# Kernel tuning notes

Hardware: AMD Instinct MI355X
Metric: run time of the kernel (lower is better)

## Reference

```python
import jax, jax.numpy as jnp
import numpy as np

B, BOUNDS, NRIM, K, UNITS = 4096, 512, 6, 4, 600
H_IN, DK_IN, DV_IN = 4, 64, 400
H_C, DK_C, DV_C = 4, 32, 100


def setup_inputs() -> dict:
    key = jax.random.key(0)
    ks = jax.random.split(key, 16)
    s = 0.02
    return {
        'inputs': jax.random.normal(ks[0], (B, BOUNDS + NRIM), jnp.float32),
        'hs': jax.random.normal(ks[1], (B, NRIM, UNITS), jnp.float32) * s,
        'cs': jax.random.normal(ks[2], (B, NRIM, UNITS), jnp.float32) * s,
        'Wk': jax.random.normal(ks[3], (BOUNDS, H_IN * DK_IN), jnp.float32) * s,
        'bk': jnp.zeros((H_IN * DK_IN,), jnp.float32),
        'Wv': jax.random.normal(ks[4], (BOUNDS, H_IN * DV_IN), jnp.float32) * s,
        'bv': jnp.zeros((H_IN * DV_IN,), jnp.float32),
        'Wq': jax.random.normal(ks[5], (NRIM, UNITS, H_IN * DK_IN), jnp.float32) * s,
        'lstm_k': jax.random.normal(ks[6], (NRIM, DV_IN, 4 * UNITS), jnp.float32) * s,
        'lstm_r': jax.random.normal(ks[7], (NRIM, UNITS, 4 * UNITS), jnp.float32) * s,
        'lstm_b': jnp.zeros((NRIM, 4 * UNITS), jnp.float32),
        'Wkc': jax.random.normal(ks[8], (NRIM, UNITS, H_C * DK_C), jnp.float32) * s,
        'Wvc': jax.random.normal(ks[9], (NRIM, UNITS, H_C * DV_C), jnp.float32) * s,
        'Wqc': jax.random.normal(ks[10], (NRIM, UNITS, H_C * DK_C), jnp.float32) * s,
        'Wout': jax.random.normal(ks[11], (NRIM, H_C * DV_C, UNITS), jnp.float32) * s,
    }


def _split_heads(t, n_heads, d_head):
    # [B, T, n_heads*d_head] -> [B, n_heads, T, d_head] (matches tf.split+stack)
    b, t_len = t.shape[0], t.shape[1]
    return t.reshape(b, t_len, n_heads, d_head).transpose(0, 2, 1, 3)


def reference(inputs, hs, cs, Wk, bk, Wv, bv, Wq, lstm_k, lstm_r, lstm_b, Wkc, Wvc, Wqc, Wout):
    x = inputs[:, :BOUNDS]                                   # [B, bounds]
    rim_dist = inputs[:, BOUNDS:BOUNDS + NRIM]               # [B, nRIM]

    # ---- input attention ----
    xx = jnp.stack([x, jnp.zeros_like(x)], axis=1)           # [B, 2, bounds]
    k_lay = xx @ Wk + bk                                     # [B, 2, H*dk]
    v_lay = xx @ Wv + bv                                     # [B, 2, H*dv]
    q_lay = jnp.einsum('bnu,nuo->bno', hs, Wq)               # grouped linear [B, nRIM, H*dq]
    kh = _split_heads(k_lay, H_IN, DK_IN)                    # [B, H, 2, dk]
    vh = _split_heads(v_lay, H_IN, DV_IN)                    # [B, H, 2, dv]
    qh = _split_heads(q_lay, H_IN, DK_IN)                    # [B, H, nRIM, dk]
    v2 = vh.mean(axis=1)                                     # [B, 2, dv]
    scores = jnp.einsum('bhnd,bhtd->bhnt', qh, kh) / np.sqrt(DK_IN).astype(np.float32)
    scores2 = scores.mean(axis=1)                            # [B, nRIM, 2]

    # top-k RIM selection mask from RIM_dist (use_attn=False path)
    _, idx = jax.lax.top_k(rim_dist, K)                      # [B, K]
    mask = jnp.zeros((inputs.shape[0], NRIM), inputs.dtype)
    mask = mask.at[jnp.arange(inputs.shape[0])[:, None], idx].set(1.0)[..., None]  # [B, nRIM, 1]

    probs = jax.nn.softmax(scores2, axis=-1)                 # dropout inactive (training=False)
    rnn_in = jnp.einsum('bnt,btv->bnv', probs, v2) * mask    # [B, nRIM, dv]

    # ---- grouped LSTM (keras gate order i,f,c,o) ----
    gates = (jnp.einsum('bnv,nvo->bno', rnn_in, lstm_k)
             + jnp.einsum('bnu,nuo->bno', hs, lstm_r) + lstm_b)  # [B, nRIM, 4*units]
    i, f, g, o = jnp.split(gates, 4, axis=-1)
    c_rnn = jax.nn.sigmoid(f) * cs + jax.nn.sigmoid(i) * jnp.tanh(g)
    h_rnn = jax.nn.sigmoid(o) * jnp.tanh(c_rnn)
    h_new = jax.lax.stop_gradient(h_rnn * (1.0 - mask)) + h_rnn * mask

    # ---- communication attention among RIMs ----
    kc = _split_heads(jnp.einsum('bnu,nuo->bno', h_new, Wkc), H_C, DK_C)  # [B, Hc, nRIM, dkc]
    vc = _split_heads(jnp.einsum('bnu,nuo->bno', h_new, Wvc), H_C, DV_C)
    qc = _split_heads(jnp.einsum('bnu,nuo->bno', h_new, Wqc), H_C, DK_C)
    sc = jnp.einsum('bhnd,bhmd->bhnm', qc, kc) / np.sqrt(DK_C).astype(np.float32)
    pc = jax.nn.softmax(sc, axis=-1) * mask[:, None, :, :]   # zero rows of inactive query RIMs
    ctx = jnp.einsum('bhnm,bhmv->bhnv', pc, vc)              # [B, Hc, nRIM, dvc]
    ctx = ctx.transpose(0, 2, 1, 3).reshape(inputs.shape[0], NRIM, H_C * DV_C)
    h_comm = jnp.einsum('bno,nou->bnu', ctx, Wout) + h_new   # grouped output proj + residual

    # ---- masked state update ----
    h_upd = h_comm * mask + hs * (1.0 - mask)
    c_upd = c_rnn * mask + cs * (1.0 - mask)
    out_state = h_upd.reshape(inputs.shape[0], UNITS * NRIM)
    return out_state, h_upd, c_upd
```

## Files before the change

kernel.cpp:

```cpp
#include <hip/hip_runtime.h>

namespace {
typedef unsigned short u16;
typedef __attribute__((ext_vector_type(8))) __bf16 bf16x8;
typedef __attribute__((ext_vector_type(4))) float f32x4;

constexpr long long kB  = 4096;
constexpr long long kOS = kB * 3600;

constexpr size_t oWkvT  = 0;
constexpr size_t oWqT   = oWkvT  + 768ull*512*2;
constexpr size_t oWcomT = oWqT   + 6ull*256*608*2;
constexpr size_t oWoutT = oWcomT + 6ull*768*608*2;
constexpr size_t oLstmT = oWoutT + 6ull*640*416*2;
constexpr size_t oBp    = oLstmT + 6ull*2432*1024*2;
constexpr size_t oBkv   = oBp    + 6ull*2432*4;
constexpr size_t oZero  = oBkv   + 768*4;
constexpr size_t oMask  = oZero  + 256;
constexpr size_t oArena = oMask  + 4096ull*6*4;
constexpr size_t oHs2   = oArena;
constexpr size_t oRnn   = oHs2  + (4096ull*3600+64)*2;
constexpr size_t oKV    = oRnn  + 4096ull*2400*2;
constexpr size_t oXbf   = oKV   + 4096ull*768*2;
constexpr size_t oQlay  = oXbf;
constexpr size_t oCqv   = oArena;
constexpr size_t oCtx   = oCqv  + 4096ull*4608*2;
}

__device__ __forceinline__ u16 f2b(float f) {
  union { float f; unsigned u; } x; x.f = f;
  unsigned r = (x.u + 0x7fffu + ((x.u >> 16) & 1u)) >> 16;
  return (u16)r;
}
__device__ __forceinline__ float b2f(u16 u) {
  union { unsigned u; float f; } x; x.u = ((unsigned)u) << 16;
  return x.f;
}
__device__ __forceinline__ float sigmoidf_(float x) { return 1.f / (1.f + __expf(-x)); }

__device__ __forceinline__ void gload16(const void* g, void* l) {
  __builtin_amdgcn_global_load_lds((const __attribute__((address_space(1))) void*)g,
                                   (__attribute__((address_space(3))) void*)l, 16, 0, 0);
}

union FragU { uint2 u2[2]; bf16x8 v; };

template<int MODE>
__global__ __launch_bounds__(256) void gemm128(
    const u16* __restrict__ A, int lda, int strideA,
    const u16* __restrict__ A2, int lda2, int strideA2,
    const u16* __restrict__ Bt, long strideB, int Kpad,
    void* __restrict__ C, int ldc, int strideC,
    const float* __restrict__ bias, int strideBias,
    int N, int nks, int storeBf16, int nx, int swz,
    const u16* __restrict__ zerobuf,
    const float* __restrict__ cs, const float* __restrict__ mask,
    float* __restrict__ c_upd, float* __restrict__ h_upd, u16* __restrict__ hnbf,
    const float* __restrict__ hs_in, float* __restrict__ out_state)
{
  __shared__ __align__(16) u16 As[128 * 32];
  __shared__ __align__(16) u16 Bs[128 * 32];

  const int nwg = gridDim.x;
  const int orig = blockIdx.x;
  const int q = nwg >> 3, r = nwg & 7;
  const int xcd = orig & 7, bidx = orig >> 3;
  const int wgid = (xcd < r ? xcd * (q + 1) : r * (q + 1) + (xcd - r) * q) + bidx;
  int xt, mt, rim;
  if (swz == 0) {
    xt = wgid % nx;
    const int t2 = wgid / nx;
    mt = t2 & 31;
    rim = t2 >> 5;
  } else {
    const int g = wgid / 320;
    const int rem = wgid % 320;
    rim = g >> 1;
    mt = rem / 10;
    xt = (g & 1) * 10 + rem % 10;
    if (xt >= 19) return;
  }
  const int m0 = mt * 128, n0 = xt * 128;

  A += (size_t)rim * strideA;
  if (MODE == 2) A2 += (size_t)rim * strideA2;
  Bt += (size_t)rim * strideB;
  if (bias) bias += (size_t)rim * strideBias;

  const int t = threadIdx.x;
  const int w = t >> 6, lane = t & 63;
  const int lrow = lane & 15, lk = lane >> 4;
  const int wr = w >> 1, wc = w & 1;

  f32x4 acc[4][4] = {};

  const int rA0 = t >> 2,         cA0 = (t & 3) ^ ((rA0 >> 1) & 3);
  const int rA1 = (t + 256) >> 2, cA1 = (t & 3) ^ ((rA1 >> 1) & 3);

  for (int s = 0; s < nks; ++s) {
    const int k0 = s * 32;
    {
      const int gk0 = k0 + cA0 * 8, gk1 = k0 + cA1 * 8;
      const u16 *p0, *p1;
      if (MODE == 2) {
        p0 = (gk0 < 400)  ? A  + (size_t)(m0 + rA0) * lda  + gk0
           : (gk0 < 1000) ? A2 + (size_t)(m0 + rA0) * lda2 + (gk0 - 400)
                          : zerobuf;
        p1 = (gk1 < 400)  ? A  + (size_t)(m0 + rA1) * lda  + gk1
           : (gk1 < 1000) ? A2 + (size_t)(m0 + rA1) * lda2 + (gk1 - 400)
                          : zerobuf;
      } else {
        p0 = A + (size_t)(m0 + rA0) * lda + gk0;
        p1 = A + (size_t)(m0 + rA1) * lda + gk1;
      }
      gload16(p0, &As[(size_t)t * 8]);
      gload16(p1, &As[(size_t)(t + 256) * 8]);
      gload16(Bt + (size_t)(n0 + rA0) * Kpad + k0 + cA0 * 8, &Bs[(size_t)t * 8]);
      gload16(Bt + (size_t)(n0 + rA1) * Kpad + k0 + cA1 * 8, &Bs[(size_t)(t + 256) * 8]);
    }
    __syncthreads();
    FragU af[4], bfr[4];
#pragma unroll
    for (int mf = 0; mf < 4; ++mf) {
      const int rr = wr * 64 + mf * 16 + lrow;
      const int sw = ((rr >> 1) & 3) << 4;
      const char* base = (const char*)As + rr * 64;
      af[mf].u2[0] = *(const uint2*)(base + ((8 * lk) ^ sw));
      af[mf].u2[1] = *(const uint2*)(base + ((8 * lk + 32) ^ sw));
    }
#pragma unroll
    for (int nf = 0; nf < 4; ++nf) {
      const int rr = wc * 64 + nf * 16 + lrow;
      const int sw = ((rr >> 1) & 3) << 4;
      const char* base = (const char*)Bs + rr * 64;
      bfr[nf].u2[0] = *(const uint2*)(base + ((8 * lk) ^ sw));
      bfr[nf].u2[1] = *(const uint2*)(base + ((8 * lk + 32) ^ sw));
    }
#pragma unroll
    for (int mf = 0; mf < 4; ++mf)
#pragma unroll
      for (int nf = 0; nf < 4; ++nf)
        acc[mf][nf] = __builtin_amdgcn_mfma_f32_16x16x32_bf16(af[mf].v, bfr[nf].v, acc[mf][nf], 0, 0, 0);
    __syncthreads();
  }

  if (MODE == 0) {
    float* Cf = (float*)C + (size_t)rim * strideC;
    u16*   Cu = (u16*)C + (size_t)rim * strideC;
#pragma unroll
    for (int mf = 0; mf < 4; ++mf)
#pragma unroll
      for (int r2 = 0; r2 < 4; ++r2) {
        const int m = m0 + wr * 64 + mf * 16 + 4 * lk + r2;
#pragma unroll
        for (int nf = 0; nf < 4; ++nf) {
          const int col = n0 + wc * 64 + nf * 16 + lrow;
          if (col < N) {
            float v = acc[mf][nf][r2];
            if (bias) v += bias[col];
            const size_t off = (size_t)m * ldc + col;
            if (storeBf16) Cu[off] = f2b(v); else Cf[off] = v;
          }
        }
      }
  } else if (MODE == 1) {
#pragma unroll
    for (int mf = 0; mf < 4; ++mf)
#pragma unroll
      for (int r2 = 0; r2 < 4; ++r2) {
        const int m = m0 + wr * 64 + mf * 16 + 4 * lk + r2;
        const float mk = mask[(size_t)m * 6 + rim];
#pragma unroll
        for (int nf = 0; nf < 4; ++nf) {
          const int col = n0 + wc * 64 + nf * 16 + lrow;
          if (col < 600) {
            const size_t off = (size_t)m * 3600 + rim * 600 + col;
            const float v = (mk != 0.f) ? (acc[mf][nf][r2] + h_upd[off]) : hs_in[off];
            h_upd[off] = v;
            out_state[off] = v;
          }
        }
      }
  } else {
    const int nb = n0 + wc * 64;
    const int u = ((nb >> 6) << 4) + lrow;
    if (u < 600) {
      const float bi  = bias[nb + lrow];
      const float bff = bias[nb + 16 + lrow];
      const float bg  = bias[nb + 32 + lrow];
      const float bo  = bias[nb + 48 + lrow];
#pragma unroll
      for (int mf = 0; mf < 4; ++mf)
#pragma unroll
        for (int r2 = 0; r2 < 4; ++r2) {
          const int m = m0 + wr * 64 + mf * 16 + 4 * lk + r2;
          const float iv = acc[mf][0][r2] + bi;
          const float fv = acc[mf][1][r2] + bff;
          const float gv = acc[mf][2][r2] + bg;
          const float ov = acc[mf][3][r2] + bo;
          const size_t off = (size_t)m * 3600 + rim * 600 + u;
          const float cprev = cs[off];
          const float cv = sigmoidf_(fv) * cprev + sigmoidf_(iv) * tanhf(gv);
          const float hv = sigmoidf_(ov) * tanhf(cv);
          const float mk = mask[(size_t)m * 6 + rim];
          c_upd[off] = (mk != 0.f) ? cv : cprev;
          h_upd[off] = hv;
          hnbf[off]  = f2b(hv);
        }
    }
  }
}

__global__ __launch_bounds__(256) void pack_wt(
    const float* __restrict__ in1, long s1,
    const float* __restrict__ in2, long s2,
    int K1, int Ktot, int ldin, int Nreal,
    u16* __restrict__ out, long so, int Kpad, int gateperm)
{
  __shared__ float tile[64][65];
  const int rim = blockIdx.z;
  const float* i1 = in1 + (size_t)rim * s1;
  const float* i2 = in2 ? in2 + (size_t)rim * s2 : nullptr;
  u16* o = out + (size_t)rim * so;
  const int n0 = blockIdx.x * 64, k0 = blockIdx.y * 64;
  const int lane = threadIdx.x & 63, qq = threadIdx.x >> 6;
  const int n = n0 + lane;
  int col;
  if (gateperm) {
    const int g = (n >> 4) & 3, u = ((n >> 6) << 4) + (n & 15);
    col = (u < 600) ? g * 600 + u : -1;
  } else {
    col = (n < Nreal) ? n : -1;
  }
#pragma unroll
  for (int i = 0; i < 16; ++i) {
    const int kk = qq + 4 * i;
    const int k = k0 + kk;
    float v = 0.f;
    if (col >= 0) {
      if (k < K1) v = i1[(size_t)k * ldin + col];
      else if (k < Ktot) v = i2[(size_t)(k - K1) * ldin + col];
    }
    tile[kk][lane] = v;
  }
  __syncthreads();
#pragma unroll
  for (int i = 0; i < 16; ++i) {
    const int nn = qq + 4 * i;
    const int k = k0 + lane;
    if (k < Kpad) o[(size_t)(n0 + nn) * Kpad + k] = f2b(tile[lane][nn]);
  }
}

__global__ void pack_kvw(const float* __restrict__ Wk, const float* __restrict__ Wv,
                         u16* __restrict__ out) {
  const int i = blockIdx.x * 256 + threadIdx.x;
  if (i >= 768 * 512) return;
  const int n = i >> 9, k = i & 511;
  float v = 0.f;
  if (n < 256) v = Wk[(size_t)k * 256 + n];
  else if (n < 656) {
    const float* p = Wv + (size_t)k * 1600 + (n - 256);
    v = 0.25f * (p[0] + p[400] + p[800] + p[1200]);
  }
  out[i] = f2b(v);
}

__global__ void pack_comw(const float* __restrict__ Wkc, const float* __restrict__ Wqc,
                          const float* __restrict__ Wvc, u16* __restrict__ out) {
  const long long i = (long long)blockIdx.x * 256 + threadIdx.x;
  if (i >= 6ll * 768 * 608) return;
  const int rim = (int)(i / (768 * 608));
  const int rem = (int)(i % (768 * 608));
  const int n = rem / 608, k = rem % 608;
  float v = 0.f;
  if (k < 600) {
    if (n < 128)      v = Wkc[(size_t)rim * 600 * 128 + (size_t)k * 128 + n];
    else if (n < 256) v = Wqc[(size_t)rim * 600 * 128 + (size_t)k * 128 + (n - 128)];
    else if (n < 656) v = Wvc[(size_t)rim * 600 * 400 + (size_t)k * 400 + (n - 256)];
  }
  out[i] = f2b(v);
}

__global__ void pack_misc(const float* __restrict__ lstm_b, const float* __restrict__ bk,
                          const float* __restrict__ bv,
                          float* __restrict__ bp, float* __restrict__ bkv, u16* __restrict__ zerobuf) {
  const int t = blockIdx.x * 256 + threadIdx.x;
  if (t < 6 * 2432) {
    const int rim = t / 2432, p = t % 2432;
    const int g = (p >> 4) & 3, u = ((p >> 6) << 4) + (p & 15);
    bp[t] = (u < 600) ? lstm_b[(size_t)rim * 2400 + g * 600 + u] : 0.f;
  }
  if (t < 768) {
    float v = 0.f;
    if (t < 256) v = bk[t];
    else if (t < 656) { const int j = t - 256; v = 0.25f * (bv[j] + bv[j + 400] + bv[j + 800] + bv[j + 1200]); }
    bkv[t] = v;
  }
  if (t < 128) zerobuf[t] = 0;
}

__global__ void pack_x(const float* __restrict__ inputs, u16* __restrict__ xbf) {
  const int idx = blockIdx.x * 256 + threadIdx.x;
  if (idx < 4096 * 512) {
    const int b = idx >> 9, c = idx & 511;
    xbf[idx] = f2b(inputs[(size_t)b * 518 + c]);
  }
}

__global__ void pack_hs2(const float* __restrict__ hs, u16* __restrict__ out) {
  const long long idx = (long long)blockIdx.x * 256 + threadIdx.x;
  const long long total = 4096ll * 3600 + 64;
  if (idx < total) out[idx] = f2b(idx < 4096ll * 3600 ? hs[idx] : 0.f);
}

__global__ __launch_bounds__(256) void score_kernel(
    const float* __restrict__ inputs, const u16* __restrict__ qlayb,
    const u16* __restrict__ kvb, const float* __restrict__ bk,
    const float* __restrict__ bkv,
    float* __restrict__ maskout, u16* __restrict__ rnnin)
{
  const int b = blockIdx.x;
  const int t = threadIdx.x;
  __shared__ float red[4][12];
  __shared__ float sprob[12];
  __shared__ float smask[6];

  const float k0v = b2f(kvb[(size_t)b * 768 + t]);
  const float bkv_ = bk[t];
  float part[12];
#pragma unroll
  for (int n = 0; n < 6; ++n) {
    const float q = b2f(qlayb[(size_t)b * 1536 + n * 256 + t]);
    part[2 * n]     = q * k0v;
    part[2 * n + 1] = q * bkv_;
  }
#pragma unroll
  for (int off = 32; off > 0; off >>= 1)
#pragma unroll
    for (int i = 0; i < 12; ++i)
      part[i] += __shfl_down(part[i], off);
  const int wave = t >> 6, lane = t & 63;
  if (lane == 0)
#pragma unroll
    for (int i = 0; i < 12; ++i) red[wave][i] = part[i];
  __syncthreads();
  if (t < 12) red[0][t] = (red[0][t] + red[1][t] + red[2][t] + red[3][t]) * (1.0f / 32.0f);
  __syncthreads();
  if (t < 6) {
    const float s0 = red[0][2 * t], s1 = red[0][2 * t + 1];
    const float mx = fmaxf(s0, s1);
    const float e0 = __expf(s0 - mx), e1 = __expf(s1 - mx);
    const float inv = 1.f / (e0 + e1);
    sprob[2 * t] = e0 * inv;
    sprob[2 * t + 1] = e1 * inv;
    const float* rd = inputs + (size_t)b * 518 + 512;
    const float mine = rd[t];
    int rank = 0;
#pragma unroll
    for (int j = 0; j < 6; ++j) {
      const float o = rd[j];
      rank += (o > mine) || (o == mine && j < t);
    }
    const float mk = (rank < 4) ? 1.f : 0.f;
    smask[t] = mk;
    maskout[(size_t)b * 6 + t] = mk;
  }
  __syncthreads();
  for (int idx = t; idx < 2400; idx += 256) {
    const int n = idx / 400, v = idx % 400;
    const float val = (sprob[2 * n] * b2f(kvb[(size_t)b * 768 + 256 + v]) + sprob[2 * n + 1] * bkv[256 + v]) * smask[n];
    rnnin[(size_t)b * 2400 + idx] = f2b(val);
  }
}

__global__ __launch_bounds__(256) void comm_kernel(
    const u16* __restrict__ cqv, u16* __restrict__ ctx)
{
  const int b = blockIdx.x, t = threadIdx.x;
  __shared__ float skc[768], sqc[768], svc[2400];
  __shared__ float spc[4][6][6];
  for (int i = t; i < 4608; i += 256) {
    const int m = i / 768, c = i % 768;
    const float v = b2f(cqv[(size_t)b * 4608 + i]);
    if (c < 128) skc[m * 128 + c] = v;
    else if (c < 256) sqc[m * 128 + (c - 128)] = v;
    else if (c < 656) svc[m * 400 + (c - 256)] = v;
  }
  __syncthreads();
  if (t < 144) {
    const int h = t / 36, n = (t % 36) / 6, m = t % 6;
    float s = 0.f;
#pragma unroll
    for (int d = 0; d < 32; ++d) s += sqc[n * 128 + h * 32 + d] * skc[m * 128 + h * 32 + d];
    spc[h][n][m] = s * 0.17677669529663687f;
  }
  __syncthreads();
  if (t < 24) {
    const int h = t / 6, n = t % 6;
    float mx = -3.0e38f;
#pragma unroll
    for (int m = 0; m < 6; ++m) mx = fmaxf(mx, spc[h][n][m]);
    float e[6], sum = 0.f;
#pragma unroll
    for (int m = 0; m < 6; ++m) { e[m] = __expf(spc[h][n][m] - mx); sum += e[m]; }
    const float inv = 1.f / sum;
#pragma unroll
    for (int m = 0; m < 6; ++m) spc[h][n][m] = e[m] * inv;
  }
  __syncthreads();
  for (int idx = t; idx < 2400; idx += 256) {
    const int n = idx / 400, rr = idx % 400, h = rr / 100, v = rr % 100;
    float s = 0.f;
#pragma unroll
    for (int m = 0; m < 6; ++m) s += spc[h][n][m] * svc[m * 400 + h * 100 + v];
    ctx[(size_t)b * 2400 + idx] = f2b(s);
  }
}

extern "C" void kernel_launch(void* const* d_in, const int* in_sizes, int n_in,
                              void* d_out, int out_size, void* d_ws, size_t ws_size,
                              hipStream_t stream) {
  const float* inputs = (const float*)d_in[0];
  const float* hs     = (const float*)d_in[1];
  const float* cs     = (const float*)d_in[2];
  const float* Wk     = (const float*)d_in[3];
  const float* bk     = (const float*)d_in[4];
  const float* Wv     = (const float*)d_in[5];
  const float* bv     = (const float*)d_in[6];
  const float* Wq     = (const float*)d_in[7];
  const float* lstm_k = (const float*)d_in[8];
  const float* lstm_r = (const float*)d_in[9];
  const float* lstm_b = (const float*)d_in[10];
  const float* Wkc    = (const float*)d_in[11];
  const float* Wvc    = (const float*)d_in[12];
  const float* Wqc    = (const float*)d_in[13];
  const float* Wout   = (const float*)d_in[14];

  float* out = (float*)d_out;
  float* out_state = out;
  float* h_upd = out + kOS;
  float* c_upd = out + 2 * kOS;
  u16*   hnbf  = (u16*)d_out;

  char* wsb = (char*)d_ws;
  u16* WkvT  = (u16*)(wsb + oWkvT);
  u16* WqT   = (u16*)(wsb + oWqT);
  u16* WcomT = (u16*)(wsb + oWcomT);
  u16* WoutT = (u16*)(wsb + oWoutT);
  u16* LstmT = (u16*)(wsb + oLstmT);
  float* bp    = (float*)(wsb + oBp);
  float* bkv   = (float*)(wsb + oBkv);
  u16*   zerob = (u16*)(wsb + oZero);
  float* maskf = (float*)(wsb + oMask);
  u16* hs2   = (u16*)(wsb + oHs2);
  u16* rnn   = (u16*)(wsb + oRnn);
  u16* kvb   = (u16*)(wsb + oKV);
  u16* xbf   = (u16*)(wsb + oXbf);
  u16* qlayb = (u16*)(wsb + oQlay);
  u16* cqvb  = (u16*)(wsb + oCqv);
  u16* ctxb  = (u16*)(wsb + oCtx);

  dim3 B256(256);

  pack_misc<<<57, B256, 0, stream>>>(lstm_b, bk, bv, bp, bkv, zerob);
  pack_kvw<<<1536, B256, 0, stream>>>(Wk, Wv, WkvT);
  pack_comw<<<10944, B256, 0, stream>>>(Wkc, Wqc, Wvc, WcomT);
  pack_wt<<<dim3(4, 10, 6), B256, 0, stream>>>(Wq, 600ll*256, nullptr, 0, 600, 600, 256, 256, WqT, 256ll*608, 608, 0);
  pack_wt<<<dim3(10, 7, 6), B256, 0, stream>>>(Wout, 400ll*600, nullptr, 0, 400, 400, 600, 600, WoutT, 640ll*416, 416, 0);
  pack_wt<<<dim3(38, 16, 6), B256, 0, stream>>>(lstm_k, 400ll*2400, lstm_r, 600ll*2400, 400, 1000, 2400, 2400, LstmT, 2432ll*1024, 1024, 1);
  pack_x<<<8192, B256, 0, stream>>>(inputs, xbf);
  pack_hs2<<<57601, B256, 0, stream>>>(hs, hs2);

  gemm128<0><<<dim3(6*32), B256, 0, stream>>>(xbf, 512, 0, nullptr, 0, 0, WkvT, 0, 512,
      kvb, 768, 0, bkv, 0, 656, 16, 1, 6, 0, zerob,
      nullptr, nullptr, nullptr, nullptr, nullptr, nullptr, nullptr);
  gemm128<0><<<dim3(2*32*6), B256, 0, stream>>>(hs2, 3600, 600, nullptr, 0, 0, WqT, 256*608, 608,
      qlayb, 1536, 256, nullptr, 0, 256, 19, 1, 2, 0, zerob,
      nullptr, nullptr, nullptr, nullptr, nullptr, nullptr, nullptr);

  score_kernel<<<4096, B256, 0, stream>>>(inputs, qlayb, kvb, bk, bkv, maskf, rnn);

  gemm128<2><<<dim3(3840), B256, 0, stream>>>(rnn, 2400, 400, hs2, 3600, 600, LstmT, 2432l*1024, 1024,
      nullptr, 0, 0, bp, 2432, 2432, 32, 0, 10, 1, zerob,
      cs, maskf, c_upd, h_upd, hnbf, nullptr, nullptr);

  gemm128<0><<<dim3(6*32*6), B256, 0, stream>>>(hnbf, 3600, 600, nullptr, 0, 0, WcomT, 768l*608, 608,
      cqvb, 4608, 768, nullptr, 0, 656, 19, 1, 6, 0, zerob,
      nullptr, nullptr, nullptr, nullptr, nullptr, nullptr, nullptr);

  comm_kernel<<<4096, B256, 0, stream>>>(cqvb, ctxb);

  gemm128<1><<<dim3(5*32*6), B256, 0, stream>>>(ctxb, 2400, 400, nullptr, 0, 0, WoutT, 640l*416, 416,
      nullptr, 0, 0, nullptr, 0, 600, 13, 0, 5, 0, zerob,
      nullptr, maskf, nullptr, h_upd, nullptr, hs, out_state);
}
```

Before: 680.1 us.

## Double-buffer GEMM LDS staging, vectorize pack/score/comm kernels, use fast tanh

The GEMM main loop now uses two LDS buffers, issuing the next K-slice's global-to-LDS loads before the MFMAs on the current slice, with an explicit vmcnt wait and barrier. This is meant to overlap memory latency with compute. Several elementwise kernels (hs bf16 packing, score output, comm attention load and ctx store) are vectorized to 4 or 8 elements per thread to cut instruction and store overhead. tanhf in the LSTM epilogue is replaced by an exp-based approximation, which is slightly less accurate and can overflow to inf for large inputs, though the formula still evaluates to 1 in that case. The extra buffers double LDS use per block, which may reduce occupancy.

```diff
diff --git a/kernel.cpp b/kernel.cpp
--- a/kernel.cpp
+++ b/kernel.cpp
@@ -37,10 +37,18 @@
   return x.f;
 }
 __device__ __forceinline__ float sigmoidf_(float x) { return 1.f / (1.f + __expf(-x)); }
+__device__ __forceinline__ float tanhf_(float x) {
+  const float e = __expf(2.f * x);
+  return 1.f - 2.f / (e + 1.f);
+}
 
 __device__ __forceinline__ void gload16(const void* g, void* l) {
   __builtin_amdgcn_global_load_lds((const __attribute__((address_space(1))) void*)g,
                                    (__attribute__((address_space(3))) void*)l, 16, 0, 0);
+}
+__device__ __forceinline__ void vmcnt0_barrier() {
+  asm volatile("s_waitcnt vmcnt(0)" ::: "memory");
+  __builtin_amdgcn_s_barrier();
 }
 
 union FragU { uint2 u2[2]; bf16x8 v; };
@@ -58,8 +66,10 @@
     float* __restrict__ c_upd, float* __restrict__ h_upd, u16* __restrict__ hnbf,
     const float* __restrict__ hs_in, float* __restrict__ out_state)
 {
-  __shared__ __align__(16) u16 As[128 * 32];
-  __shared__ __align__(16) u16 Bs[128 * 32];
+  __shared__ __align__(16) u16 As0[128 * 32];
+  __shared__ __align__(16) u16 Bs0[128 * 32];
+  __shared__ __align__(16) u16 As1[128 * 32];
+  __shared__ __align__(16) u16 Bs1[128 * 32];
 
   const int nwg = gridDim.x;
   const int orig = blockIdx.x;
@@ -97,34 +107,34 @@
   const int rA0 = t >> 2,         cA0 = (t & 3) ^ ((rA0 >> 1) & 3);
   const int rA1 = (t + 256) >> 2, cA1 = (t & 3) ^ ((rA1 >> 1) & 3);
 
-  for (int s = 0; s < nks; ++s) {
+  auto stage = [&](int s, u16* Asd, u16* Bsd) {
     const int k0 = s * 32;
-    {
-      const int gk0 = k0 + cA0 * 8, gk1 = k0 + cA1 * 8;
-      const u16 *p0, *p1;
-      if (MODE == 2) {
-        p0 = (gk0 < 400)  ? A  + (size_t)(m0 + rA0) * lda  + gk0
-           : (gk0 < 1000) ? A2 + (size_t)(m0 + rA0) * lda2 + (gk0 - 400)
-                          : zerobuf;
-        p1 = (gk1 < 400)  ? A  + (size_t)(m0 + rA1) * lda  + gk1
-           : (gk1 < 1000) ? A2 + (size_t)(m0 + rA1) * lda2 + (gk1 - 400)
-                          : zerobuf;
-      } else {
-        p0 = A + (size_t)(m0 + rA0) * lda + gk0;
-        p1 = A + (size_t)(m0 + rA1) * lda + gk1;
-      }
-      gload16(p0, &As[(size_t)t * 8]);
-      gload16(p1, &As[(size_t)(t + 256) * 8]);
-      gload16(Bt + (size_t)(n0 + rA0) * Kpad + k0 + cA0 * 8, &Bs[(size_t)t * 8]);
-      gload16(Bt + (size_t)(n0 + rA1) * Kpad + k0 + cA1 * 8, &Bs[(size_t)(t + 256) * 8]);
-    }
-    __syncthreads();
+    const int gk0 = k0 + cA0 * 8, gk1 = k0 + cA1 * 8;
+    const u16 *p0, *p1;
+    if (MODE == 2) {
+      p0 = (gk0 < 400)  ? A  + (size_t)(m0 + rA0) * lda  + gk0
+         : (gk0 < 1000) ? A2 + (size_t)(m0 + rA0) * lda2 + (gk0 - 400)
+                        : zerobuf;
+      p1 = (gk1 < 400)  ? A  + (size_t)(m0 + rA1) * lda  + gk1
+         : (gk1 < 1000) ? A2 + (size_t)(m0 + rA1) * lda2 + (gk1 - 400)
+                        : zerobuf;
+    } else {
+      p0 = A + (size_t)(m0 + rA0) * lda + gk0;
+      p1 = A + (size_t)(m0 + rA1) * lda + gk1;
+    }
+    gload16(p0, Asd + (size_t)t * 8);
+    gload16(p1, Asd + (size_t)(t + 256) * 8);
+    gload16(Bt + (size_t)(n0 + rA0) * Kpad + k0 + cA0 * 8, Bsd + (size_t)t * 8);
+    gload16(Bt + (size_t)(n0 + rA1) * Kpad + k0 + cA1 * 8, Bsd + (size_t)(t + 256) * 8);
+  };
+
+  auto compute = [&](const u16* Asrc, const u16* Bsrc, int snext, u16* Asd, u16* Bsd, bool donext) {
     FragU af[4], bfr[4];
 #pragma unroll
     for (int mf = 0; mf < 4; ++mf) {
       const int rr = wr * 64 + mf * 16 + lrow;
       const int sw = ((rr >> 1) & 3) << 4;
-      const char* base = (const char*)As + rr * 64;
+      const char* base = (const char*)Asrc + rr * 64;
       af[mf].u2[0] = *(const uint2*)(base + ((8 * lk) ^ sw));
       af[mf].u2[1] = *(const uint2*)(base + ((8 * lk + 32) ^ sw));
     }
@@ -132,17 +142,27 @@
     for (int nf = 0; nf < 4; ++nf) {
       const int rr = wc * 64 + nf * 16 + lrow;
       const int sw = ((rr >> 1) & 3) << 4;
-      const char* base = (const char*)Bs + rr * 64;
+      const char* base = (const char*)Bsrc + rr * 64;
       bfr[nf].u2[0] = *(const uint2*)(base + ((8 * lk) ^ sw));
       bfr[nf].u2[1] = *(const uint2*)(base + ((8 * lk + 32) ^ sw));
     }
+    if (donext) stage(snext, Asd, Bsd);
 #pragma unroll
     for (int mf = 0; mf < 4; ++mf)
 #pragma unroll
       for (int nf = 0; nf < 4; ++nf)
         acc[mf][nf] = __builtin_amdgcn_mfma_f32_16x16x32_bf16(af[mf].v, bfr[nf].v, acc[mf][nf], 0, 0, 0);
-    __syncthreads();
-  }
+    vmcnt0_barrier();
+  };
+
+  stage(0, As0, Bs0);
+  vmcnt0_barrier();
+  int s = 0;
+  for (; s + 2 <= nks; s += 2) {
+    compute(As0, Bs0, s + 1, As1, Bs1, s + 1 < nks);
+    compute(As1, Bs1, s + 2, As0, Bs0, s + 2 < nks);
+  }
+  if (s < nks) compute(As0, Bs0, 0, As1, Bs1, false);
 
   if (MODE == 0) {
     float* Cf = (float*)C + (size_t)rim * strideC;
@@ -200,8 +220,8 @@
           const float ov = acc[mf][3][r2] + bo;
           const size_t off = (size_t)m * 3600 + rim * 600 + u;
           const float cprev = cs[off];
-          const float cv = sigmoidf_(fv) * cprev + sigmoidf_(iv) * tanhf(gv);
-          const float hv = sigmoidf_(ov) * tanhf(cv);
+          const float cv = sigmoidf_(fv) * cprev + sigmoidf_(iv) * tanhf_(gv);
+          const float hv = sigmoidf_(ov) * tanhf_(cv);
           const float mk = mask[(size_t)m * 6 + rim];
           c_upd[off] = (mk != 0.f) ? cv : cprev;
           h_upd[off] = hv;
@@ -309,9 +329,20 @@
 }
 
 __global__ void pack_hs2(const float* __restrict__ hs, u16* __restrict__ out) {
-  const long long idx = (long long)blockIdx.x * 256 + threadIdx.x;
-  const long long total = 4096ll * 3600 + 64;
-  if (idx < total) out[idx] = f2b(idx < 4096ll * 3600 ? hs[idx] : 0.f);
+  const long long i8 = ((long long)blockIdx.x * 256 + threadIdx.x) * 8;
+  const long long main_n = 4096ll * 3600;
+  if (i8 + 8 <= main_n) {
+    const float4 a = *reinterpret_cast<const float4*>(hs + i8);
+    const float4 b = *reinterpret_cast<const float4*>(hs + i8 + 4);
+    u16 r[8] = {f2b(a.x), f2b(a.y), f2b(a.z), f2b(a.w), f2b(b.x), f2b(b.y), f2b(b.z), f2b(b.w)};
+    *reinterpret_cast<uint4*>(out + i8) = *reinterpret_cast<const uint4*>(r);
+  } else if (i8 < main_n + 64) {
+#pragma unroll
+    for (int j = 0; j < 8; ++j) {
+      const long long idx = i8 + j;
+      if (idx < main_n + 64) out[idx] = f2b(idx < main_n ? hs[idx] : 0.f);
+    }
+  }
 }
 
 __global__ __launch_bounds__(256) void score_kernel(
@@ -367,10 +398,15 @@
     maskout[(size_t)b * 6 + t] = mk;
   }
   __syncthreads();
-  for (int idx = t; idx < 2400; idx += 256) {
-    const int n = idx / 400, v = idx % 400;
-    const float val = (sprob[2 * n] * b2f(kvb[(size_t)b * 768 + 256 + v]) + sprob[2 * n + 1] * bkv[256 + v]) * smask[n];
-    rnnin[(size_t)b * 2400 + idx] = f2b(val);
+  for (int base = t * 4; base < 2400; base += 1024) {
+    const int n = base / 400, v = base % 400;
+    const float p0 = sprob[2 * n], p1 = sprob[2 * n + 1], mk = smask[n];
+    ushort4 st;
+    st.x = f2b((p0 * b2f(kvb[(size_t)b * 768 + 256 + v + 0]) + p1 * bkv[256 + v + 0]) * mk);
+    st.y = f2b((p0 * b2f(kvb[(size_t)b * 768 + 256 + v + 1]) + p1 * bkv[256 + v + 1]) * mk);
+    st.z = f2b((p0 * b2f(kvb[(size_t)b * 768 + 256 + v + 2]) + p1 * bkv[256 + v + 2]) * mk);
+    st.w = f2b((p0 * b2f(kvb[(size_t)b * 768 + 256 + v + 3]) + p1 * bkv[256 + v + 3]) * mk);
+    *reinterpret_cast<ushort4*>(rnnin + (size_t)b * 2400 + base) = st;
   }
 }
 
@@ -380,12 +416,18 @@
   const int b = blockIdx.x, t = threadIdx.x;
   __shared__ float skc[768], sqc[768], svc[2400];
   __shared__ float spc[4][6][6];
-  for (int i = t; i < 4608; i += 256) {
-    const int m = i / 768, c = i % 768;
-    const float v = b2f(cqv[(size_t)b * 4608 + i]);
-    if (c < 128) skc[m * 128 + c] = v;
-    else if (c < 256) sqc[m * 128 + (c - 128)] = v;
-    else if (c < 656) svc[m * 400 + (c - 256)] = v;
+  for (int i = t * 4; i < 4608; i += 1024) {
+    const ushort4 u4 = *reinterpret_cast<const ushort4*>(cqv + (size_t)b * 4608 + i);
+    const u16 uu[4] = {u4.x, u4.y, u4.z, u4.w};
+#pragma unroll
+    for (int j = 0; j < 4; ++j) {
+      const int ii = i + j;
+      const int m = ii / 768, c = ii % 768;
+      const float v = b2f(uu[j]);
+      if (c < 128) skc[m * 128 + c] = v;
+      else if (c < 256) sqc[m * 128 + (c - 128)] = v;
+      else if (c < 656) svc[m * 400 + (c - 256)] = v;
+    }
   }
   __syncthreads();
   if (t < 144) {
@@ -409,12 +451,18 @@
     for (int m = 0; m < 6; ++m) spc[h][n][m] = e[m] * inv;
   }
   __syncthreads();
-  for (int idx = t; idx < 2400; idx += 256) {
-    const int n = idx / 400, rr = idx % 400, h = rr / 100, v = rr % 100;
-    float s = 0.f;
-#pragma unroll
-    for (int m = 0; m < 6; ++m) s += spc[h][n][m] * svc[m * 400 + h * 100 + v];
-    ctx[(size_t)b * 2400 + idx] = f2b(s);
+  for (int base = t * 4; base < 2400; base += 1024) {
+    const int n = base / 400, rr = base % 400, h = rr / 100, v = rr % 100;
+    ushort4 st;
+    float s0 = 0.f, s1 = 0.f, s2 = 0.f, s3 = 0.f;
+#pragma unroll
+    for (int m = 0; m < 6; ++m) {
+      const float p = spc[h][n][m];
+      const float* vm = &svc[m * 400 + h * 100 + v];
+      s0 += p * vm[0]; s1 += p * vm[1]; s2 += p * vm[2]; s3 += p * vm[3];
+    }
+    st.x = f2b(s0); st.y = f2b(s1); st.z = f2b(s2); st.w = f2b(s3);
+    *reinterpret_cast<ushort4*>(ctx + (size_t)b * 2400 + base) = st;
   }
 }
 
@@ -470,7 +518,7 @@
   pack_wt<<<dim3(10, 7, 6), B256, 0, stream>>>(Wout, 400ll*600, nullptr, 0, 400, 400, 600, 600, WoutT, 640ll*416, 416, 0);
   pack_wt<<<dim3(38, 16, 6), B256, 0, stream>>>(lstm_k, 400ll*2400, lstm_r, 600ll*2400, 400, 1000, 2400, 2400, LstmT, 2432ll*1024, 1024, 1);
   pack_x<<<8192, B256, 0, stream>>>(inputs, xbf);
-  pack_hs2<<<57601, B256, 0, stream>>>(hs, hs2);
+  pack_hs2<<<7201, B256, 0, stream>>>(hs, hs2);
 
   gemm128<0><<<dim3(6*32), B256, 0, stream>>>(xbf, 512, 0, nullptr, 0, 0, WkvT, 0, 512,
       kvb, 768, 0, bkv, 0, 656, 16, 1, 6, 0, zerob,
```

Measured after the change: 701.4 us. +3.1%, slower.
